# Optimization experiments

Measured on AMD Instinct MI355X. Metric: run time of the kernel, lower is better.

The kernel has to match this reference:

```python
import jax, jax.numpy as jnp
import numpy as np

B = 256
D = 2048          # in_channels (shared latent dim)
S = 8             # n_subjects
OUT = 1000        # sum of 7 Schaefer network head widths [150,148,132,136,76,122,236]


def setup_inputs() -> dict:
    key = jax.random.key(0)
    k1, k2, k3, k4 = jax.random.split(key, 4)
    x = jax.random.normal(k1, (B, D), dtype=jnp.float32)
    subject_ids = jax.random.randint(k2, (B,), 0, S, dtype=jnp.int64)
    scale = 1.0 / np.sqrt(D)  # matches normal_(0, 1/in_channels**0.5)
    # Concatenated per-head weights: equivalent to 7 heads of shapes
    # (S, D, n_k) concatenated along the output axis (n_k sums to OUT).
    W = jax.random.normal(k3, (S, D, OUT), dtype=jnp.float32) * scale
    b = jax.random.normal(k4, (S, OUT), dtype=jnp.float32) * scale
    return {"x": x, "subject_ids": subject_ids, "W": W, "b": b}


def reference(x, subject_ids, W, b):
    # Per-sample weight gather (B, D, OUT) followed by batched matmul,
    # exactly mirroring torch: w = weights[subject_ids]; einsum('bd,bdo->bo').
    w = W[subject_ids]                      # (B, D, OUT) gathered copy
    out = jnp.einsum('bd,bdo->bo', x, w)    # (B, OUT)
    out = out + b[subject_ids]              # per-subject bias
    return out
```

## Files before the change

kernel.cpp:

```cpp
#include <hip/hip_runtime.h>
#include <stdint.h>

#define Bn   256
#define Dn   2048
#define Sn   8
#define ON   1000

#define ROWS 64
#define OT   64
#define KC   256
#define NDC  (Dn / KC)
#define NCH  (KC / 32)
#define NIT  (KC / 32)
#define LDK  (KC + 8)

typedef short v8s __attribute__((ext_vector_type(8)));
typedef float v4f __attribute__((ext_vector_type(4)));

static __device__ __forceinline__ short f2bf(float f) {
    union { float f; uint32_t u; } v; v.f = f;
    uint32_t u = v.u;
    u += 0x7FFFu + ((u >> 16) & 1u);
    return (short)(u >> 16);
}

__global__ __launch_bounds__(256) void gather_kernel(const float* __restrict__ x,
                                                     const int* __restrict__ sid,
                                                     unsigned short* __restrict__ xg) {
    __shared__ unsigned long long bmask[4];
    __shared__ int brow;
    const int r = blockIdx.x;
    const int s = blockIdx.y;
    const int t = threadIdx.x;
    const int lane = t & 63;
    const int wave = t >> 6;

    const bool match = (sid[t] == s);
    const unsigned long long m = __ballot(match);
    if (lane == 0) bmask[wave] = m;
    if (t == 0) brow = -1;
    __syncthreads();
    if (match) {
        int pos = __popcll(m & ((1ull << lane) - 1ull));
        for (int w = 0; w < wave; ++w) pos += __popcll(bmask[w]);
        if (pos == r) brow = t;
    }
    __syncthreads();

    const int b = brow;
    v8s v = (v8s){0, 0, 0, 0, 0, 0, 0, 0};
    if (b >= 0) {
        const float4 f0 = *(const float4*)(x + (size_t)b * Dn + t * 8);
        const float4 f1 = *(const float4*)(x + (size_t)b * Dn + t * 8 + 4);
        v[0] = f2bf(f0.x); v[1] = f2bf(f0.y); v[2] = f2bf(f0.z); v[3] = f2bf(f0.w);
        v[4] = f2bf(f1.x); v[5] = f2bf(f1.y); v[6] = f2bf(f1.z); v[7] = f2bf(f1.w);
    }
    *(v8s*)(xg + ((size_t)s * ROWS + r) * Dn + t * 8) = v;
}

__global__ __launch_bounds__(256, 4) void main_kernel(const unsigned short* __restrict__ xg,
                                                      const int* __restrict__ sid,
                                                      const float* __restrict__ W,
                                                      float* __restrict__ part) {
    __shared__ unsigned short Bsh[OT * LDK];
    __shared__ unsigned long long bmask[4];
    __shared__ int rows_l[ROWS];

    const int oc = blockIdx.x;
    const int dc = blockIdx.y;
    const int s  = blockIdx.z;
    const int o0 = oc * OT;
    const int d0 = dc * KC;
    const int t  = threadIdx.x;
    const int lane = t & 63;
    const int wave = t >> 6;

    const int mysid = sid[t];
    const bool match = (mysid == s);
    const unsigned long long m = __ballot(match);
    if (lane == 0) bmask[wave] = m;
    if (t < ROWS) rows_l[t] = -1;
    __syncthreads();
    if (match) {
        int pos = __popcll(m & ((1ull << lane) - 1ull));
        for (int w = 0; w < wave; ++w) pos += __popcll(bmask[w]);
        if (pos < ROWS) rows_l[pos] = t;
    }
    __syncthreads();

    int og = o0 + lane; if (og > ON - 1) og = ON - 1;
    const float* wp = W + (size_t)s * Dn * ON + (size_t)(d0 + wave * 8) * ON + og;
    const int boff0 = lane * LDK + wave * 8;

    float fb[2][8];
#pragma unroll
    for (int c = 0; c < 2; ++c)
#pragma unroll
        for (int j = 0; j < 8; ++j) fb[c][j] = wp[(size_t)(c * 32 + j) * ON];

    const int lo16 = lane & 15;
    const int quad = lane >> 4;
    const int ar   = wave * 16 + lo16;
    const unsigned short* xr = xg + ((size_t)s * ROWS + ar) * Dn + d0 + quad * 8;
    v8s af[NIT];
#pragma unroll
    for (int it = 0; it < NIT; ++it) af[it] = *(const v8s*)(xr + it * 32);

#pragma unroll
    for (int c = 0; c < NCH; ++c) {
        const int sl = c & 1;
        v8s bv;
#pragma unroll
        for (int j = 0; j < 8; ++j) bv[j] = f2bf(fb[sl][j]);
        *(v8s*)&Bsh[boff0 + c * 32] = bv;
        if (c + 2 < NCH) {
#pragma unroll
            for (int j = 0; j < 8; ++j) fb[sl][j] = wp[(size_t)((c + 2) * 32 + j) * ON];
        }
    }

    __syncthreads();

    v4f acc[4];
#pragma unroll
    for (int i = 0; i < 4; i++) acc[i] = (v4f){0.f, 0.f, 0.f, 0.f};

#pragma unroll
    for (int it = 0; it < NIT; ++it) {
#pragma unroll
        for (int nt = 0; nt < 4; nt++) {
            const v8s bf = *(const v8s*)&Bsh[(nt * 16 + lo16) * LDK + it * 32 + quad * 8];
            acc[nt] = __builtin_amdgcn_mfma_f32_16x16x32_bf16(af[it], bf, acc[nt], 0, 0, 0);
        }
    }

    float* pp = part + (size_t)dc * Bn * ON;
    const int er0 = wave * 16 + quad * 4;
#pragma unroll
    for (int nt = 0; nt < 4; nt++) {
        const int o = o0 + nt * 16 + lo16;
        if (o < ON) {
#pragma unroll
            for (int r = 0; r < 4; r++) {
                const int bi = rows_l[er0 + r];
                if (bi >= 0) pp[(size_t)bi * ON + o] = acc[nt][r];
            }
        }
    }
}

__global__ __launch_bounds__(256) void reduce_kernel(const int* __restrict__ sid,
                                                     const float* __restrict__ bias,
                                                     const float* __restrict__ part,
                                                     float* __restrict__ out) {
    const int b = blockIdx.x;
    const int s = sid[b];
    const int o = threadIdx.x * 4;
    if (o < ON) {
        float4 v = *(const float4*)(bias + (size_t)s * ON + o);
#pragma unroll
        for (int d = 0; d < NDC; d++) {
            const float4 p = *(const float4*)(part + ((size_t)d * Bn + b) * ON + o);
            v.x += p.x; v.y += p.y; v.z += p.z; v.w += p.w;
        }
        *(float4*)(out + (size_t)b * ON + o) = v;
    }
}

extern "C" void kernel_launch(void* const* d_in, const int* in_sizes, int n_in,
                              void* d_out, int out_size, void* d_ws, size_t ws_size,
                              hipStream_t stream) {
    const float* x    = (const float*)d_in[0];
    const int*   sid  = (const int*)d_in[1];
    const float* W    = (const float*)d_in[2];
    const float* bias = (const float*)d_in[3];
    float*       out  = (float*)d_out;
    float*       part = (float*)d_ws;
    unsigned short* xg = (unsigned short*)((char*)d_ws + (size_t)NDC * Bn * ON * sizeof(float));

    gather_kernel<<<dim3(ROWS, Sn), dim3(256), 0, stream>>>(x, sid, xg);
    main_kernel<<<dim3(16, NDC, Sn), dim3(256), 0, stream>>>(xg, sid, W, part);
    reduce_kernel<<<dim3(Bn), dim3(256), 0, stream>>>(sid, bias, part, out);
}
```

Baseline: 110.8 us.

## Widen output tile to 256 with 512 threads, vectorized W loads, double-buffered swizzled LDS

Restructures the main GEMM kernel so each 512-thread block covers 256 output columns. W is loaded with float4 vector reads, which gives wider global transactions. The K dimension is streamed in 32-wide stages through a double-buffered, XOR-swizzled LDS tile, so conversion and stores can overlap MFMA work under one barrier per stage. Waves whose 16-row group holds no valid samples skip the MFMAs and the stores. In exchange, the grid shrinks to 256 blocks and a barrier is added in every stage.

Result: no change. 108.7 us (-1.9%).

```diff
diff --git a/kernel.cpp b/kernel.cpp
--- a/kernel.cpp
+++ b/kernel.cpp
@@ -7,14 +7,16 @@
 #define ON   1000
 
 #define ROWS 64
-#define OT   64
-#define KC   256
-#define NDC  (Dn / KC)
-#define NCH  (KC / 32)
-#define NIT  (KC / 32)
-#define LDK  (KC + 8)
+#define OT   256
+#define KS   256
+#define NDC  (Dn / KS)
+#define STK  32
+#define NST  (KS / STK)
+#define LDKS 40
+#define BUFB (OT * LDKS * 2)
 
 typedef short v8s __attribute__((ext_vector_type(8)));
+typedef short v4s __attribute__((ext_vector_type(4)));
 typedef float v4f __attribute__((ext_vector_type(4)));
 
 static __device__ __forceinline__ short f2bf(float f) {
@@ -58,92 +60,115 @@
     *(v8s*)(xg + ((size_t)s * ROWS + r) * Dn + t * 8) = v;
 }
 
-__global__ __launch_bounds__(256, 4) void main_kernel(const unsigned short* __restrict__ xg,
-                                                      const int* __restrict__ sid,
-                                                      const float* __restrict__ W,
-                                                      float* __restrict__ part) {
-    __shared__ unsigned short Bsh[OT * LDK];
-    __shared__ unsigned long long bmask[4];
+__global__ __launch_bounds__(512) void main_kernel(const unsigned short* __restrict__ xg,
+                                                   const int* __restrict__ sid,
+                                                   const float* __restrict__ W,
+                                                   float* __restrict__ part) {
+    __shared__ unsigned short Bsh[2][OT * LDKS];
+    __shared__ unsigned long long bmask[8];
     __shared__ int rows_l[ROWS];
 
     const int oc = blockIdx.x;
-    const int dc = blockIdx.y;
+    const int kc = blockIdx.y;
     const int s  = blockIdx.z;
     const int o0 = oc * OT;
-    const int d0 = dc * KC;
+    const int k0 = kc * KS;
     const int t  = threadIdx.x;
     const int lane = t & 63;
-    const int wave = t >> 6;
-
-    const int mysid = sid[t];
+    const int w    = t >> 6;
+
+    const int mysid = (t < Bn) ? sid[t] : -1;
     const bool match = (mysid == s);
     const unsigned long long m = __ballot(match);
-    if (lane == 0) bmask[wave] = m;
+    if (lane == 0) bmask[w] = m;
     if (t < ROWS) rows_l[t] = -1;
     __syncthreads();
     if (match) {
         int pos = __popcll(m & ((1ull << lane) - 1ull));
-        for (int w = 0; w < wave; ++w) pos += __popcll(bmask[w]);
+        for (int ww = 0; ww < w; ++ww) pos += __popcll(bmask[ww]);
         if (pos < ROWS) rows_l[pos] = t;
     }
     __syncthreads();
 
-    int og = o0 + lane; if (og > ON - 1) og = ON - 1;
-    const float* wp = W + (size_t)s * Dn * ON + (size_t)(d0 + wave * 8) * ON + og;
-    const int boff0 = lane * LDK + wave * 8;
-
-    float fb[2][8];
-#pragma unroll
-    for (int c = 0; c < 2; ++c)
-#pragma unroll
-        for (int j = 0; j < 8; ++j) fb[c][j] = wp[(size_t)(c * 32 + j) * ON];
+    int og = o0 + 4 * lane;
+    if (og > ON - 4) og = ON - 4;
+    const float* wpb = W + ((size_t)s * Dn + k0 + 4 * w) * ON + og;
+
+    unsigned short* wr[4];
+#pragma unroll
+    for (int i = 0; i < 4; ++i)
+        wr[i] = (unsigned short*)((char*)&Bsh[0][0]
+                + (4 * lane + i) * 80 + 16 * ((w >> 1) ^ (lane & 3)) + 8 * (w & 1));
 
     const int lo16 = lane & 15;
     const int quad = lane >> 4;
-    const int ar   = wave * 16 + lo16;
-    const unsigned short* xr = xg + ((size_t)s * ROWS + ar) * Dn + d0 + quad * 8;
-    v8s af[NIT];
-#pragma unroll
-    for (int it = 0; it < NIT; ++it) af[it] = *(const v8s*)(xr + it * 32);
-
-#pragma unroll
-    for (int c = 0; c < NCH; ++c) {
-        const int sl = c & 1;
-        v8s bv;
-#pragma unroll
-        for (int j = 0; j < 8; ++j) bv[j] = f2bf(fb[sl][j]);
-        *(v8s*)&Bsh[boff0 + c * 32] = bv;
-        if (c + 2 < NCH) {
-#pragma unroll
-            for (int j = 0; j < 8; ++j) fb[sl][j] = wp[(size_t)((c + 2) * 32 + j) * ON];
-        }
-    }
-
-    __syncthreads();
-
-    v4f acc[4];
-#pragma unroll
-    for (int i = 0; i < 4; i++) acc[i] = (v4f){0.f, 0.f, 0.f, 0.f};
-
-#pragma unroll
-    for (int it = 0; it < NIT; ++it) {
-#pragma unroll
-        for (int nt = 0; nt < 4; nt++) {
-            const v8s bf = *(const v8s*)&Bsh[(nt * 16 + lo16) * LDK + it * 32 + quad * 8];
-            acc[nt] = __builtin_amdgcn_mfma_f32_16x16x32_bf16(af[it], bf, acc[nt], 0, 0, 0);
-        }
-    }
-
-    float* pp = part + (size_t)dc * Bn * ON;
-    const int er0 = wave * 16 + quad * 4;
-#pragma unroll
-    for (int nt = 0; nt < 4; nt++) {
-        const int o = o0 + nt * 16 + lo16;
-        if (o < ON) {
-#pragma unroll
-            for (int r = 0; r < 4; r++) {
-                const int bi = rows_l[er0 + r];
-                if (bi >= 0) pp[(size_t)bi * ON + o] = acc[nt][r];
+    const int arow = (w >> 1) * 16 + lo16;
+    const bool wactive = (rows_l[(w >> 1) * 16] >= 0);
+    const unsigned short* xr = xg + ((size_t)s * ROWS + arow) * Dn + k0 + quad * 8;
+
+    v8s af[NST];
+#pragma unroll
+    for (int st = 0; st < NST; ++st) af[st] = *(const v8s*)(xr + st * STK);
+
+    const int rb0  = (w & 1) * 128 + lo16;
+    const int rswz = 16 * (quad ^ ((lo16 >> 2) & 3));
+
+    v4f fb[2][4];
+#pragma unroll
+    for (int c = 0; c < 2; ++c)
+#pragma unroll
+        for (int r = 0; r < 4; ++r)
+            fb[c][r] = *(const v4f*)(wpb + ((size_t)c * STK + r) * ON);
+
+    v4f acc[8];
+#pragma unroll
+    for (int i = 0; i < 8; ++i) acc[i] = (v4f){0.f, 0.f, 0.f, 0.f};
+
+#pragma unroll
+    for (int st = 0; st < NST; ++st) {
+        const int sl = st & 1;
+#pragma unroll
+        for (int i = 0; i < 4; ++i) {
+            v4s kv;
+            kv[0] = f2bf(fb[sl][0][i]);
+            kv[1] = f2bf(fb[sl][1][i]);
+            kv[2] = f2bf(fb[sl][2][i]);
+            kv[3] = f2bf(fb[sl][3][i]);
+            *(v4s*)((char*)wr[i] + sl * BUFB) = kv;
+        }
+        if (st + 2 < NST) {
+#pragma unroll
+            for (int r = 0; r < 4; ++r)
+                fb[sl][r] = *(const v4f*)(wpb + ((size_t)(st + 2) * STK + r) * ON);
+        }
+        asm volatile("s_waitcnt lgkmcnt(0)" ::: "memory");
+        __builtin_amdgcn_s_barrier();
+        asm volatile("" ::: "memory");
+
+        if (wactive) {
+            const v8s a = af[st];
+            const char* bb = (const char*)&Bsh[sl][0];
+#pragma unroll
+            for (int nt = 0; nt < 8; ++nt) {
+                const v8s bf = *(const v8s*)(bb + (rb0 + nt * 16) * 80 + rswz);
+                acc[nt] = __builtin_amdgcn_mfma_f32_16x16x32_bf16(a, bf, acc[nt],
+                                                                  0, 0, 0);
+            }
+        }
+    }
+
+    if (wactive) {
+        float* pp = part + (size_t)kc * Bn * ON;
+        const int er0 = (w >> 1) * 16 + quad * 4;
+#pragma unroll
+        for (int nt = 0; nt < 8; ++nt) {
+            const int o = o0 + (w & 1) * 128 + nt * 16 + lo16;
+            if (o < ON) {
+#pragma unroll
+                for (int r = 0; r < 4; ++r) {
+                    const int bi = rows_l[er0 + r];
+                    if (bi >= 0) pp[(size_t)bi * ON + o] = acc[nt][r];
+                }
             }
         }
     }
@@ -179,6 +204,6 @@
     unsigned short* xg = (unsigned short*)((char*)d_ws + (size_t)NDC * Bn * ON * sizeof(float));
 
     gather_kernel<<<dim3(ROWS, Sn), dim3(256), 0, stream>>>(x, sid, xg);
-    main_kernel<<<dim3(16, NDC, Sn), dim3(256), 0, stream>>>(xg, sid, W, part);
+    main_kernel<<<dim3(4, NDC, Sn), dim3(512), 0, stream>>>(xg, sid, W, part);
     reduce_kernel<<<dim3(Bn), dim3(256), 0, stream>>>(sid, bias, part, out);
 }
```
